# Optimization experiments

Measured on AMD Instinct MI355X. Metric: run time of the kernel, lower is better.

## Reference

```python
import jax, jax.numpy as jnp
import numpy as np
import jax.lax as lax

EPS_VAR = 1e-05  # hardcoded in original _get_statistics sqrt(var + 1e-05)


def _get_statistics(x):
    # x: (B, P, L). Cumulative NaN-aware mean/std along patch dim P.
    B, P, L = x.shape
    nan_mask = jnp.isnan(x)
    nan_counts = jnp.cumsum(nan_mask.sum(-1, keepdims=True).astype(x.dtype), axis=1)  # (B,P,1)
    counts = (jnp.arange(1, P + 1, dtype=x.dtype).reshape(1, P, 1)) * L - nan_counts   # (B,P,1)
    x0 = jnp.where(nan_mask, jnp.zeros_like(x), x)
    cumsum_x = jnp.cumsum(x0.sum(-1, keepdims=True), axis=1)          # nansum then cumsum
    mean = cumsum_x / counts
    cumsum_x2 = jnp.cumsum((x0 * x0).sum(-1, keepdims=True), axis=1)  # nansum of x^2
    var = (cumsum_x2 - 2.0 * mean * cumsum_x + counts * mean * mean) / counts
    std = jnp.sqrt(var + EPS_VAR)
    return mean, std


def _fill_nan_with_last_observed(x):
    # x: (B, P, L); forward-fill NaNs along last axis per (b,p) row.
    L = x.shape[-1]
    valid_mask = ~jnp.isnan(x)
    x_temp = jnp.where(valid_mask, x, jnp.zeros_like(x))
    seq_idx = jnp.arange(L, dtype=jnp.int32)
    valid_idx = jnp.where(valid_mask, seq_idx, jnp.int32(-1))
    last_valid = lax.cummax(valid_idx, axis=x.ndim - 1)
    return jnp.take_along_axis(x_temp, jnp.clip(last_valid, 0, None), axis=-1)


def setup_inputs() -> dict:
    key = jax.random.key(0)
    x = jax.random.normal(key, (128, 1024, 128), dtype=jnp.float32)
    return {"x": x}


def reference(x):
    # RevIN forward, mode='norm' (fresh cache). Original upcasts to float64;
    # we keep the input dtype (fp32) for kernel-comparison purposes.
    mean, std = _get_statistics(x)
    out = (x - mean) / std
    out = _fill_nan_with_last_observed(out)  # identity when no NaNs present
    return out.astype(jnp.float32)
```

## Files before the change

### kernel.cpp

```cpp
#include <hip/hip_runtime.h>
#include <math.h>

#define BB 128
#define PP 1024
#define LL 128
#define NROWS (BB * PP)
#define EPS_VAR 1e-5f
#define NBLK 1024
#define ROWS_PER_BLK 128
#define CHUNKS 8

typedef float vfloat4 __attribute__((ext_vector_type(4)));

__device__ __forceinline__ bool is_nan_bits(float f) {
    return (__float_as_uint(f) & 0x7fffffffu) > 0x7f800000u;
}

__global__ __launch_bounds__(256) void k_chunktot(const float* __restrict__ x,
                                                  float4* __restrict__ tot) {
    __shared__ float ws1[4], ws2[4], wsc[4];
    const int g = blockIdx.x;
    const int t = threadIdx.x;
    const int lane = t & 63;
    const int wav  = t >> 6;

    const vfloat4* px = (const vfloat4*)(x + (size_t)g * (ROWS_PER_BLK * LL));

    float s1 = 0.f, s2 = 0.f, c = 0.f;
#pragma unroll
    for (int i = 0; i < 16; ++i) {
        const vfloat4 v = px[t + 256 * i];
#pragma unroll
        for (int j = 0; j < 4; ++j) {
            const float f = v[j];
            const bool nn = is_nan_bits(f);
            const float u = nn ? 0.f : f;
            s1 += u; s2 += u * u; c += nn ? 1.f : 0.f;
        }
    }
#pragma unroll
    for (int off = 32; off >= 1; off >>= 1) {
        s1 += __shfl_xor(s1, off);
        s2 += __shfl_xor(s2, off);
        c  += __shfl_xor(c,  off);
    }
    if (lane == 0) { ws1[wav] = s1; ws2[wav] = s2; wsc[wav] = c; }
    __syncthreads();
    if (t == 0) {
        tot[g] = make_float4(ws1[0] + ws1[1] + ws1[2] + ws1[3],
                             ws2[0] + ws2[1] + ws2[2] + ws2[3],
                             wsc[0] + wsc[1] + wsc[2] + wsc[3], 0.f);
    }
}

__device__ __attribute__((noinline)) void slow_row(const float* __restrict__ x,
                                                   float* __restrict__ out,
                                                   size_t base, int sl,
                                                   float mean, float istd,
                                                   float4 vv) {
    const float vf[4] = {vv.x, vv.y, vv.z, vv.w};
    for (int j = 0; j < 4; ++j) {
        const int l = sl * 4 + j;
        if (!is_nan_bits(vf[j])) {
            out[base + l] = (vf[j] - mean) * istd;
        } else {
            float res = 0.0f;
            for (int k = l - 1; k >= 0; --k) {
                const float xv = x[base + k];
                if (!is_nan_bits(xv)) { res = (xv - mean) * istd; break; }
            }
            out[base + l] = res;
        }
    }
}

__global__ __launch_bounds__(256, 4) void k_scan_norm(const float* __restrict__ x,
                                                      const float4* __restrict__ tot,
                                                      float* __restrict__ out) {
    __shared__ float ls1[ROWS_PER_BLK], ls2[ROWS_PER_BLK], lsc[ROWS_PER_BLK];
    __shared__ float wtot[3];
    __shared__ float off_s[3];

    const int g     = blockIdx.x;
    const int b     = g >> 3;
    const int chunk = g & 7;
    const int t     = threadIdx.x;
    const int sl    = t & 31;
    const int h     = t >> 5;
    const int p0    = chunk * ROWS_PER_BLK;
    const size_t rowbase = (size_t)b * PP + p0;

    float4 v[16];
#pragma unroll
    for (int i = 0; i < 16; ++i) {
        const int r = h + 8 * i;
        v[i] = ((const float4*)(x + (rowbase + r) * LL))[sl];
    }
#pragma unroll
    for (int i = 0; i < 16; ++i) {
        const int r = h + 8 * i;
        const float f[4] = {v[i].x, v[i].y, v[i].z, v[i].w};
        float s1 = 0.f, s2 = 0.f, c = 0.f;
#pragma unroll
        for (int j = 0; j < 4; ++j) {
            const bool nn = is_nan_bits(f[j]);
            const float u = nn ? 0.f : f[j];
            s1 += u; s2 += u * u; c += nn ? 1.f : 0.f;
        }
#pragma unroll
        for (int off = 16; off >= 1; off >>= 1) {
            s1 += __shfl_xor(s1, off);
            s2 += __shfl_xor(s2, off);
            c  += __shfl_xor(c,  off);
        }
        if (sl == 0) { ls1[r] = s1; ls2[r] = s2; lsc[r] = c; }
    }
    __syncthreads();

    const int lane = t & 63;
    float a1 = 0.f, a2 = 0.f, ac = 0.f;
    if (t < 128) { a1 = ls1[t]; a2 = ls2[t]; ac = lsc[t]; }
#pragma unroll
    for (int off = 1; off < 64; off <<= 1) {
        const float u1 = __shfl_up(a1, off);
        const float u2 = __shfl_up(a2, off);
        const float u3 = __shfl_up(ac, off);
        if (lane >= off) { a1 += u1; a2 += u2; ac += u3; }
    }
    if (t == 63) { wtot[0] = a1; wtot[1] = a2; wtot[2] = ac; }
    __syncthreads();
    if (t >= 64 && t < 128) { a1 += wtot[0]; a2 += wtot[1]; ac += wtot[2]; }
    if (t < 128) { ls1[t] = a1; ls2[t] = a2; lsc[t] = ac; }

    if (t == 0) {
        float o1 = 0.f, o2 = 0.f, oc = 0.f;
        for (int j = 0; j < chunk; ++j) {
            const float4 ct = tot[(b << 3) + j];
            o1 += ct.x; o2 += ct.y; oc += ct.z;
        }
        off_s[0] = o1; off_s[1] = o2; off_s[2] = oc;
    }
    __syncthreads();
    const float o1 = off_s[0], o2 = off_s[1], oc = off_s[2];

#pragma unroll
    for (int i = 0; i < 16; ++i) {
        const int r = h + 8 * i;
        const float cum1 = o1 + ls1[r];
        const float cum2 = o2 + ls2[r];
        const float cumc = oc + lsc[r];
        const int p = p0 + r;
        const float cnt  = (float)((p + 1) * LL) - cumc;
        const float mean = cum1 / cnt;
        const float var  = cum2 / cnt - mean * mean;
        const float istd = 1.0f / sqrtf(var + EPS_VAR);
        const float4 vv = v[i];
        const size_t base = (rowbase + r) * (size_t)LL;

        const bool anynan = is_nan_bits(vv.x) | is_nan_bits(vv.y) |
                            is_nan_bits(vv.z) | is_nan_bits(vv.w);
        if (__ballot(anynan) == 0ull) {
            vfloat4 y = {(vv.x - mean) * istd, (vv.y - mean) * istd,
                         (vv.z - mean) * istd, (vv.w - mean) * istd};
            __builtin_nontemporal_store(y, &((vfloat4*)(out + base))[sl]);
        } else {
            slow_row(x, out, base, sl, mean, istd, vv);
        }
    }
}

extern "C" void kernel_launch(void* const* d_in, const int* in_sizes, int n_in,
                              void* d_out, int out_size, void* d_ws, size_t ws_size,
                              hipStream_t stream) {
    const float* x = (const float*)d_in[0];
    float* outp = (float*)d_out;
    float4* tot = (float4*)d_ws;

    k_chunktot<<<NBLK, 256, 0, stream>>>(x, tot);
    k_scan_norm<<<NBLK, 256, 0, stream>>>(x, tot, outp);
}
```

Before: 135.2 us.

## Precompute per-row stats in first pass; drop register-held slab in scan kernel

The first kernel now writes each row's sum, sum of squares and NaN count to workspace, alongside the per-chunk totals. The second kernel reads these row stats instead of recomputing them. It no longer holds all 16 float4s in registers and loads x lazily inside the normalize loop. Chunk prefix totals are loaded in parallel into shared memory instead of by a serial thread-0 loop. The intent is to cut register pressure and reduction work in the scan kernel, at the cost of extra workspace traffic (about 2 MB) and an extra barrier.

```diff
diff --git a/kernel.cpp b/kernel.cpp
--- a/kernel.cpp
+++ b/kernel.cpp
@@ -16,41 +16,59 @@
     return (__float_as_uint(f) & 0x7fffffffu) > 0x7f800000u;
 }
 
-__global__ __launch_bounds__(256) void k_chunktot(const float* __restrict__ x,
-                                                  float4* __restrict__ tot) {
+__global__ __launch_bounds__(256) void k_chunkstats(const float* __restrict__ x,
+                                                    float4* __restrict__ rowstats,
+                                                    float4* __restrict__ chunkTot) {
+    __shared__ float4 lrow[ROWS_PER_BLK];
     __shared__ float ws1[4], ws2[4], wsc[4];
-    const int g = blockIdx.x;
-    const int t = threadIdx.x;
+
+    const int g    = blockIdx.x;
+    const int t    = threadIdx.x;
+    const int sl   = t & 31;
+    const int h    = t >> 5;
     const int lane = t & 63;
     const int wav  = t >> 6;
 
-    const vfloat4* px = (const vfloat4*)(x + (size_t)g * (ROWS_PER_BLK * LL));
+    const float* slab = x + (size_t)g * (ROWS_PER_BLK * LL);
 
-    float s1 = 0.f, s2 = 0.f, c = 0.f;
+    float c1 = 0.f, c2 = 0.f, cc = 0.f;
 #pragma unroll
     for (int i = 0; i < 16; ++i) {
-        const vfloat4 v = px[t + 256 * i];
+        const int r = h + 8 * i;
+        const float4 v = ((const float4*)(slab + (size_t)r * LL))[sl];
+        const float f[4] = {v.x, v.y, v.z, v.w};
+        float s1 = 0.f, s2 = 0.f, c = 0.f;
 #pragma unroll
         for (int j = 0; j < 4; ++j) {
-            const float f = v[j];
-            const bool nn = is_nan_bits(f);
-            const float u = nn ? 0.f : f;
+            const bool nn = is_nan_bits(f[j]);
+            const float u = nn ? 0.f : f[j];
             s1 += u; s2 += u * u; c += nn ? 1.f : 0.f;
         }
+        c1 += s1; c2 += s2; cc += c;
+#pragma unroll
+        for (int off = 16; off >= 1; off >>= 1) {
+            s1 += __shfl_xor(s1, off);
+            s2 += __shfl_xor(s2, off);
+            c  += __shfl_xor(c,  off);
+        }
+        if (sl == 0) lrow[r] = make_float4(s1, s2, c, 0.f);
     }
+
 #pragma unroll
     for (int off = 32; off >= 1; off >>= 1) {
-        s1 += __shfl_xor(s1, off);
-        s2 += __shfl_xor(s2, off);
-        c  += __shfl_xor(c,  off);
+        c1 += __shfl_xor(c1, off);
+        c2 += __shfl_xor(c2, off);
+        cc += __shfl_xor(cc, off);
     }
-    if (lane == 0) { ws1[wav] = s1; ws2[wav] = s2; wsc[wav] = c; }
+    if (lane == 0) { ws1[wav] = c1; ws2[wav] = c2; wsc[wav] = cc; }
     __syncthreads();
-    if (t == 0) {
-        tot[g] = make_float4(ws1[0] + ws1[1] + ws1[2] + ws1[3],
-                             ws2[0] + ws2[1] + ws2[2] + ws2[3],
-                             wsc[0] + wsc[1] + wsc[2] + wsc[3], 0.f);
-    }
+
+    if (t < ROWS_PER_BLK)
+        rowstats[(size_t)g * ROWS_PER_BLK + t] = lrow[t];
+    if (t == 0)
+        chunkTot[g] = make_float4(ws1[0] + ws1[1] + ws1[2] + ws1[3],
+                                  ws2[0] + ws2[1] + ws2[2] + ws2[3],
+                                  wsc[0] + wsc[1] + wsc[2] + wsc[3], 0.f);
 }
 
 __device__ __attribute__((noinline)) void slow_row(const float* __restrict__ x,
@@ -74,12 +92,13 @@
     }
 }
 
-__global__ __launch_bounds__(256, 4) void k_scan_norm(const float* __restrict__ x,
-                                                      const float4* __restrict__ tot,
-                                                      float* __restrict__ out) {
+__global__ __launch_bounds__(256) void k_scan_norm(const float* __restrict__ x,
+                                                   const float4* __restrict__ rowstats,
+                                                   const float4* __restrict__ chunkTot,
+                                                   float* __restrict__ out) {
     __shared__ float ls1[ROWS_PER_BLK], ls2[ROWS_PER_BLK], lsc[ROWS_PER_BLK];
     __shared__ float wtot[3];
-    __shared__ float off_s[3];
+    __shared__ float4 pre[CHUNKS];
 
     const int g     = blockIdx.x;
     const int b     = g >> 3;
@@ -87,39 +106,15 @@
     const int t     = threadIdx.x;
     const int sl    = t & 31;
     const int h     = t >> 5;
+    const int lane  = t & 63;
     const int p0    = chunk * ROWS_PER_BLK;
     const size_t rowbase = (size_t)b * PP + p0;
 
-    float4 v[16];
-#pragma unroll
-    for (int i = 0; i < 16; ++i) {
-        const int r = h + 8 * i;
-        v[i] = ((const float4*)(x + (rowbase + r) * LL))[sl];
+    float a1 = 0.f, a2 = 0.f, ac = 0.f;
+    if (t < ROWS_PER_BLK) {
+        const float4 rs = rowstats[(size_t)g * ROWS_PER_BLK + t];
+        a1 = rs.x; a2 = rs.y; ac = rs.z;
     }
-#pragma unroll
-    for (int i = 0; i < 16; ++i) {
-        const int r = h + 8 * i;
-        const float f[4] = {v[i].x, v[i].y, v[i].z, v[i].w};
-        float s1 = 0.f, s2 = 0.f, c = 0.f;
-#pragma unroll
-        for (int j = 0; j < 4; ++j) {
-            const bool nn = is_nan_bits(f[j]);
-            const float u = nn ? 0.f : f[j];
-            s1 += u; s2 += u * u; c += nn ? 1.f : 0.f;
-        }
-#pragma unroll
-        for (int off = 16; off >= 1; off >>= 1) {
-            s1 += __shfl_xor(s1, off);
-            s2 += __shfl_xor(s2, off);
-            c  += __shfl_xor(c,  off);
-        }
-        if (sl == 0) { ls1[r] = s1; ls2[r] = s2; lsc[r] = c; }
-    }
-    __syncthreads();
-
-    const int lane = t & 63;
-    float a1 = 0.f, a2 = 0.f, ac = 0.f;
-    if (t < 128) { a1 = ls1[t]; a2 = ls2[t]; ac = lsc[t]; }
 #pragma unroll
     for (int off = 1; off < 64; off <<= 1) {
         const float u1 = __shfl_up(a1, off);
@@ -128,24 +123,24 @@
         if (lane >= off) { a1 += u1; a2 += u2; ac += u3; }
     }
     if (t == 63) { wtot[0] = a1; wtot[1] = a2; wtot[2] = ac; }
+    if (t < chunk) pre[t] = chunkTot[(b << 3) + t];
     __syncthreads();
     if (t >= 64 && t < 128) { a1 += wtot[0]; a2 += wtot[1]; ac += wtot[2]; }
-    if (t < 128) { ls1[t] = a1; ls2[t] = a2; lsc[t] = ac; }
+    if (t < ROWS_PER_BLK) { ls1[t] = a1; ls2[t] = a2; lsc[t] = ac; }
+    __syncthreads();
 
-    if (t == 0) {
-        float o1 = 0.f, o2 = 0.f, oc = 0.f;
-        for (int j = 0; j < chunk; ++j) {
-            const float4 ct = tot[(b << 3) + j];
-            o1 += ct.x; o2 += ct.y; oc += ct.z;
-        }
-        off_s[0] = o1; off_s[1] = o2; off_s[2] = oc;
+    float o1 = 0.f, o2 = 0.f, oc = 0.f;
+#pragma unroll
+    for (int j = 0; j < CHUNKS - 1; ++j) {
+        if (j < chunk) { o1 += pre[j].x; o2 += pre[j].y; oc += pre[j].z; }
     }
-    __syncthreads();
-    const float o1 = off_s[0], o2 = off_s[1], oc = off_s[2];
 
 #pragma unroll
     for (int i = 0; i < 16; ++i) {
         const int r = h + 8 * i;
+        const size_t base = (rowbase + r) * (size_t)LL;
+        const float4 vv = ((const float4*)(x + base))[sl];
+
         const float cum1 = o1 + ls1[r];
         const float cum2 = o2 + ls2[r];
         const float cumc = oc + lsc[r];
@@ -154,8 +149,6 @@
         const float mean = cum1 / cnt;
         const float var  = cum2 / cnt - mean * mean;
         const float istd = 1.0f / sqrtf(var + EPS_VAR);
-        const float4 vv = v[i];
-        const size_t base = (rowbase + r) * (size_t)LL;
 
         const bool anynan = is_nan_bits(vv.x) | is_nan_bits(vv.y) |
                             is_nan_bits(vv.z) | is_nan_bits(vv.w);
@@ -174,8 +167,10 @@
                               hipStream_t stream) {
     const float* x = (const float*)d_in[0];
     float* outp = (float*)d_out;
-    float4* tot = (float4*)d_ws;
 
-    k_chunktot<<<NBLK, 256, 0, stream>>>(x, tot);
-    k_scan_norm<<<NBLK, 256, 0, stream>>>(x, tot, outp);
+    float4* rowstats = (float4*)d_ws;
+    float4* chunkTot = (float4*)((char*)d_ws + (size_t)NROWS * sizeof(float4));
+
+    k_chunkstats<<<NBLK, 256, 0, stream>>>(x, rowstats, chunkTot);
+    k_scan_norm<<<NBLK, 256, 0, stream>>>(x, rowstats, chunkTot, outp);
 }
```

Result: faster. 129.8 us (-4.0%).
